# Performance work log

Hardware: AMD Instinct MI355X
Metric: run time of the kernel (lower is better)

Reference implementation:

```python
import jax, jax.numpy as jnp
import numpy as np

B, L, D = 16, 2048, 64

def setup_inputs() -> dict:
    key = jax.random.key(0)
    kq, kk, kv = jax.random.split(key, 3)
    q = jax.random.normal(kq, (B, L, D), dtype=jnp.float32)
    k = jax.random.normal(kk, (B, L, D), dtype=jnp.float32)
    v = jax.random.normal(kv, (B, L, D), dtype=jnp.float32)
    return {"q": q, "k": k, "v": v}

def reference(q, k, v):
    # scores: [B, L_q, L_k] = q @ k^T  (no scale applied, faithful to source)
    scores = jnp.einsum("bqd,bkd->bqk", q, k)
    attention = jax.nn.softmax(scores, axis=2)
    # dropout p=0.0 -> identity
    # source returns (v, attention), NOT the context
    return (v, attention)
```

## Files before the change

kernel.cpp:

```cpp
#include <hip/hip_runtime.h>
#include <hip/hip_bf16.h>

typedef short s16x8 __attribute__((ext_vector_type(8)));
typedef float f32x4 __attribute__((ext_vector_type(4)));

#define B_ 16
#define L_ 2048
#define D_ 64
#define V_ELEMS (B_ * L_ * D_)
#define MFMA16 __builtin_amdgcn_mfma_f32_16x16x32_bf16

__device__ __forceinline__ unsigned rne1(float f) {
    unsigned u = __builtin_bit_cast(unsigned, f);
    return (u + 0x7FFFu + ((u >> 16) & 1u)) >> 16;
}
__device__ __forceinline__ unsigned pack2(float a, float b) {
    return (rne1(a) & 0xFFFFu) | (rne1(b) << 16);
}
__device__ __forceinline__ unsigned cvtpk(float a, float b) {
    unsigned r;
    asm("v_cvt_pk_bf16_f32 %0, %1, %2" : "=v"(r) : "v"(a), "v"(b));
    return r;
}

__device__ __forceinline__ void split8(float4 a, float4 b, s16x8& hi, s16x8& lo) {
    float f[8] = {a.x, a.y, a.z, a.w, b.x, b.y, b.z, b.w};
    s16x8 h, l;
#pragma unroll
    for (int i = 0; i < 8; ++i) {
        unsigned u = __builtin_bit_cast(unsigned, f[i]);
        h[i] = (short)(u >> 16);
        float lf = f[i] - __builtin_bit_cast(float, u & 0xFFFF0000u);
        l[i] = (short)rne1(lf);
    }
    hi = h; lo = l;
}

__global__ void copy_v_kernel(const float4* __restrict__ v, float4* __restrict__ o) {
    int i = blockIdx.x * blockDim.x + threadIdx.x;
    o[i] = v[i];
}

__global__ void prep_qkv_kernel(const float4* __restrict__ q, const float4* __restrict__ k,
                                const float4* __restrict__ v,
                                uint2* __restrict__ qhi, uint2* __restrict__ qlo,
                                uint2* __restrict__ khi, uint2* __restrict__ klo,
                                float4* __restrict__ o) {
    int i = blockIdx.x * blockDim.x + threadIdx.x;
    o[i] = v[i];
    float4 fq = q[i];
    float4 fk = k[i];
    unsigned u0 = __builtin_bit_cast(unsigned, fq.x), u1 = __builtin_bit_cast(unsigned, fq.y);
    unsigned u2 = __builtin_bit_cast(unsigned, fq.z), u3 = __builtin_bit_cast(unsigned, fq.w);
    qhi[i] = make_uint2((u0 >> 16) | (u1 & 0xFFFF0000u), (u2 >> 16) | (u3 & 0xFFFF0000u));
    qlo[i] = make_uint2(
        pack2(fq.x - __builtin_bit_cast(float, u0 & 0xFFFF0000u),
              fq.y - __builtin_bit_cast(float, u1 & 0xFFFF0000u)),
        pack2(fq.z - __builtin_bit_cast(float, u2 & 0xFFFF0000u),
              fq.w - __builtin_bit_cast(float, u3 & 0xFFFF0000u)));
    u0 = __builtin_bit_cast(unsigned, fk.x); u1 = __builtin_bit_cast(unsigned, fk.y);
    u2 = __builtin_bit_cast(unsigned, fk.z); u3 = __builtin_bit_cast(unsigned, fk.w);
    khi[i] = make_uint2((u0 >> 16) | (u1 & 0xFFFF0000u), (u2 >> 16) | (u3 & 0xFFFF0000u));
    klo[i] = make_uint2(
        pack2(fk.x - __builtin_bit_cast(float, u0 & 0xFFFF0000u),
              fk.y - __builtin_bit_cast(float, u1 & 0xFFFF0000u)),
        pack2(fk.z - __builtin_bit_cast(float, u2 & 0xFFFF0000u),
              fk.w - __builtin_bit_cast(float, u3 & 0xFFFF0000u)));
}

__device__ __forceinline__ void store4nt(float* p, unsigned u0, unsigned u1, float inv) {
    f32x4 w;
    w[0] = __builtin_bit_cast(float, u0 << 16) * inv;
    w[1] = __builtin_bit_cast(float, u0 & 0xFFFF0000u) * inv;
    w[2] = __builtin_bit_cast(float, u1 << 16) * inv;
    w[3] = __builtin_bit_cast(float, u1 & 0xFFFF0000u) * inv;
    __builtin_nontemporal_store(w, (f32x4*)p);
}

template <bool PRE>
__global__ __launch_bounds__(1024, 4) void attn_kernel(
    const float* __restrict__ qf, const float* __restrict__ kf,
    const ushort* __restrict__ qhi, const ushort* __restrict__ qlo,
    const ushort* __restrict__ khi, const ushort* __restrict__ klo,
    float* __restrict__ og) {
    const int bid  = ((blockIdx.x & 7) << 7) | (blockIdx.x >> 3);
    const int b    = bid >> 6;
    const int q0   = (bid & 63) << 5;
    const int tid  = threadIdx.x;
    const int wave = tid >> 6;
    const int lane = tid & 63;
    const int nq   = lane & 15;
    const int quad = lane >> 4;

    s16x8 bhi[2][2], blo[2][2];
#pragma unroll
    for (int t = 0; t < 2; ++t) {
        const size_t off = ((size_t)(b * L_ + q0 + t * 16 + nq)) * D_ + quad * 8;
        if constexpr (PRE) {
            bhi[t][0] = *(const s16x8*)(qhi + off);
            bhi[t][1] = *(const s16x8*)(qhi + off + 32);
            blo[t][0] = *(const s16x8*)(qlo + off);
            blo[t][1] = *(const s16x8*)(qlo + off + 32);
        } else {
            float4 a0 = *(const float4*)(qf + off), a1 = *(const float4*)(qf + off + 4);
            float4 a2 = *(const float4*)(qf + off + 32), a3 = *(const float4*)(qf + off + 36);
            split8(a0, a1, bhi[t][0], blo[t][0]);
            split8(a2, a3, bhi[t][1], blo[t][1]);
        }
    }

    const size_t kbase = ((size_t)(b * L_ + wave * 128 + nq)) * D_ + quad * 8;
    const size_t tstep = (size_t)16 * D_;

    float s0 = 0.0f, s1 = 0.0f;
    unsigned pk0[16], pk1[16];

    s16x8 ah0, ah1, al0, al1;
    if constexpr (PRE) {
        ah0 = *(const s16x8*)(khi + kbase);
        ah1 = *(const s16x8*)(khi + kbase + 32);
        al0 = *(const s16x8*)(klo + kbase);
        al1 = *(const s16x8*)(klo + kbase + 32);
    } else {
        float4 a0 = *(const float4*)(kf + kbase), a1 = *(const float4*)(kf + kbase + 4);
        float4 a2 = *(const float4*)(kf + kbase + 32), a3 = *(const float4*)(kf + kbase + 36);
        split8(a0, a1, ah0, al0);
        split8(a2, a3, ah1, al1);
    }

#pragma unroll
    for (int t = 0; t < 8; ++t) {
        const size_t noff = kbase + (size_t)((t + 1) & 7) * tstep;
        s16x8 nh0, nh1, nl0, nl1;
        if constexpr (PRE) {
            nh0 = *(const s16x8*)(khi + noff);
            nh1 = *(const s16x8*)(khi + noff + 32);
            nl0 = *(const s16x8*)(klo + noff);
            nl1 = *(const s16x8*)(klo + noff + 32);
        } else {
            float4 a0 = *(const float4*)(kf + noff), a1 = *(const float4*)(kf + noff + 4);
            float4 a2 = *(const float4*)(kf + noff + 32), a3 = *(const float4*)(kf + noff + 36);
            split8(a0, a1, nh0, nl0);
            split8(a2, a3, nh1, nl1);
        }

        f32x4 c0 = {0.f, 0.f, 0.f, 0.f}, c1 = {0.f, 0.f, 0.f, 0.f};
        c0 = MFMA16(ah0, bhi[0][0], c0, 0, 0, 0);
        c1 = MFMA16(ah0, bhi[1][0], c1, 0, 0, 0);
        c0 = MFMA16(ah1, bhi[0][1], c0, 0, 0, 0);
        c1 = MFMA16(ah1, bhi[1][1], c1, 0, 0, 0);
        c0 = MFMA16(ah0, blo[0][0], c0, 0, 0, 0);
        c1 = MFMA16(ah0, blo[1][0], c1, 0, 0, 0);
        c0 = MFMA16(ah1, blo[0][1], c0, 0, 0, 0);
        c1 = MFMA16(ah1, blo[1][1], c1, 0, 0, 0);
        c0 = MFMA16(al0, bhi[0][0], c0, 0, 0, 0);
        c1 = MFMA16(al0, bhi[1][0], c1, 0, 0, 0);
        c0 = MFMA16(al1, bhi[0][1], c0, 0, 0, 0);
        c1 = MFMA16(al1, bhi[1][1], c1, 0, 0, 0);

        float e0 = __expf(c0[0]), e1 = __expf(c0[1]), e2 = __expf(c0[2]), e3 = __expf(c0[3]);
        s0 += (e0 + e1) + (e2 + e3);
        pk0[2 * t]     = cvtpk(e0, e1);
        pk0[2 * t + 1] = cvtpk(e2, e3);
        float g0 = __expf(c1[0]), g1 = __expf(c1[1]), g2 = __expf(c1[2]), g3 = __expf(c1[3]);
        s1 += (g0 + g1) + (g2 + g3);
        pk1[2 * t]     = cvtpk(g0, g1);
        pk1[2 * t + 1] = cvtpk(g2, g3);

        ah0 = nh0; ah1 = nh1; al0 = nl0; al1 = nl1;
    }

    s0 += __shfl_xor(s0, 16); s0 += __shfl_xor(s0, 32);
    s1 += __shfl_xor(s1, 16); s1 += __shfl_xor(s1, 32);
    __shared__ float wsum[16][2][16];
    if (lane < 16) { wsum[wave][0][lane] = s0; wsum[wave][1][lane] = s1; }
    __syncthreads();
    float t0 = 0.f, t1 = 0.f;
#pragma unroll
    for (int w = 0; w < 16; ++w) { t0 += wsum[w][0][nq]; t1 += wsum[w][1][nq]; }
    const float inv0 = 1.0f / t0;
    const float inv1 = 1.0f / t1;

    float* op0 = og + ((size_t)(b * L_ + q0 + nq)) * L_ + wave * 128 + quad * 4;
    float* op1 = op0 + (size_t)16 * L_;
#pragma unroll
    for (int t = 0; t < 8; ++t) {
        store4nt(op0 + t * 16, pk0[2 * t], pk0[2 * t + 1], inv0);
        store4nt(op1 + t * 16, pk1[2 * t], pk1[2 * t + 1], inv1);
    }
}

extern "C" void kernel_launch(void* const* d_in, const int* in_sizes, int n_in,
                              void* d_out, int out_size, void* d_ws, size_t ws_size,
                              hipStream_t stream) {
    const float* q = (const float*)d_in[0];
    const float* k = (const float*)d_in[1];
    const float* v = (const float*)d_in[2];
    float* out = (float*)d_out;

    float* att = out + (size_t)V_ELEMS;
    const size_t plane = (size_t)V_ELEMS;
    const size_t need  = 4 * plane * sizeof(ushort);
    ushort* qhi = (ushort*)d_ws;
    ushort* qlo = qhi + plane;
    ushort* khi = qlo + plane;
    ushort* klo = khi + plane;

    if (ws_size >= need) {
        prep_qkv_kernel<<<dim3(V_ELEMS / 4 / 256), dim3(256), 0, stream>>>(
            (const float4*)q, (const float4*)k, (const float4*)v,
            (uint2*)qhi, (uint2*)qlo, (uint2*)khi, (uint2*)klo, (float4*)out);
        attn_kernel<true><<<dim3(B_ * (L_ / 32)), dim3(1024), 0, stream>>>(
            q, k, qhi, qlo, khi, klo, att);
    } else {
        copy_v_kernel<<<dim3(V_ELEMS / 4 / 256), dim3(256), 0, stream>>>(
            (const float4*)v, (float4*)out);
        attn_kernel<false><<<dim3(B_ * (L_ / 32)), dim3(1024), 0, stream>>>(
            q, k, qhi, qlo, khi, klo, att);
    }
}
```

Baseline: 385.7 us.

## Stage packed softmax scores in LDS for coalesced row-contiguous output stores

The precomputed-split path now computes each 16-query half tile separately, writes the bf16-packed exponentials into a swizzled LDS stash, and then has the block write whole contiguous output rows with nontemporal float4 stores. Before, each lane wrote strided 16-byte pieces across rows. The aim is better coalescing on the 256MB attention output write, which is the dominant cost. In exchange, K is loaded twice (once per half tile), there are extra syncthreads and 128KB of LDS, and occupancy may drop.

New measurement: 404.5 us. 1.05x slower.

```diff
diff --git a/kernel.cpp b/kernel.cpp
--- a/kernel.cpp
+++ b/kernel.cpp
@@ -77,9 +77,7 @@
     __builtin_nontemporal_store(w, (f32x4*)p);
 }
 
-template <bool PRE>
-__global__ __launch_bounds__(1024, 4) void attn_kernel(
-    const float* __restrict__ qf, const float* __restrict__ kf,
+__global__ __launch_bounds__(1024, 4) void attn_lds_kernel(
     const ushort* __restrict__ qhi, const ushort* __restrict__ qlo,
     const ushort* __restrict__ khi, const ushort* __restrict__ klo,
     float* __restrict__ og) {
@@ -92,36 +90,113 @@
     const int nq   = lane & 15;
     const int quad = lane >> 4;
 
+    __shared__ unsigned stash[2][16][1024];
+    __shared__ float wsum[16][16];
+    __shared__ float inv_s[16];
+
     s16x8 bhi[2][2], blo[2][2];
 #pragma unroll
     for (int t = 0; t < 2; ++t) {
         const size_t off = ((size_t)(b * L_ + q0 + t * 16 + nq)) * D_ + quad * 8;
-        if constexpr (PRE) {
-            bhi[t][0] = *(const s16x8*)(qhi + off);
-            bhi[t][1] = *(const s16x8*)(qhi + off + 32);
-            blo[t][0] = *(const s16x8*)(qlo + off);
-            blo[t][1] = *(const s16x8*)(qlo + off + 32);
-        } else {
-            float4 a0 = *(const float4*)(qf + off), a1 = *(const float4*)(qf + off + 4);
-            float4 a2 = *(const float4*)(qf + off + 32), a3 = *(const float4*)(qf + off + 36);
-            split8(a0, a1, bhi[t][0], blo[t][0]);
-            split8(a2, a3, bhi[t][1], blo[t][1]);
-        }
+        bhi[t][0] = *(const s16x8*)(qhi + off);
+        bhi[t][1] = *(const s16x8*)(qhi + off + 32);
+        blo[t][0] = *(const s16x8*)(qlo + off);
+        blo[t][1] = *(const s16x8*)(qlo + off + 32);
     }
 
     const size_t kbase = ((size_t)(b * L_ + wave * 128 + nq)) * D_ + quad * 8;
     const size_t tstep = (size_t)16 * D_;
 
+    const int w3 = wave >> 3;
+    const int c4 = tid & 511;
+
+#pragma unroll
+    for (int tt = 0; tt < 2; ++tt) {
+        s16x8 ah0 = *(const s16x8*)(khi + kbase);
+        s16x8 ah1 = *(const s16x8*)(khi + kbase + 32);
+        s16x8 al0 = *(const s16x8*)(klo + kbase);
+        s16x8 al1 = *(const s16x8*)(klo + kbase + 32);
+
+        float s0 = 0.0f;
+#pragma unroll
+        for (int t = 0; t < 8; ++t) {
+            const size_t noff = kbase + (size_t)((t + 1) & 7) * tstep;
+            s16x8 nh0 = *(const s16x8*)(khi + noff);
+            s16x8 nh1 = *(const s16x8*)(khi + noff + 32);
+            s16x8 nl0 = *(const s16x8*)(klo + noff);
+            s16x8 nl1 = *(const s16x8*)(klo + noff + 32);
+
+            f32x4 c0 = {0.f, 0.f, 0.f, 0.f};
+            c0 = MFMA16(ah0, bhi[tt][0], c0, 0, 0, 0);
+            c0 = MFMA16(ah1, bhi[tt][1], c0, 0, 0, 0);
+            c0 = MFMA16(ah0, blo[tt][0], c0, 0, 0, 0);
+            c0 = MFMA16(ah1, blo[tt][1], c0, 0, 0, 0);
+            c0 = MFMA16(al0, bhi[tt][0], c0, 0, 0, 0);
+            c0 = MFMA16(al1, bhi[tt][1], c0, 0, 0, 0);
+
+            float e0 = __expf(c0[0]), e1 = __expf(c0[1]);
+            float e2 = __expf(c0[2]), e3 = __expf(c0[3]);
+            s0 += (e0 + e1) + (e2 + e3);
+            unsigned byteoff = ((unsigned)(wave * 64 + t * 8 + quad * 2) * 4u)
+                               ^ ((unsigned)nq << 3);
+            *(uint2*)((char*)&stash[tt][nq][0] + byteoff) =
+                make_uint2(cvtpk(e0, e1), cvtpk(e2, e3));
+
+            ah0 = nh0; ah1 = nh1; al0 = nl0; al1 = nl1;
+        }
+
+        s0 += __shfl_xor(s0, 16); s0 += __shfl_xor(s0, 32);
+        if (lane < 16) wsum[wave][nq] = s0;
+        __syncthreads();
+        if (tid < 16) {
+            float t0 = 0.f;
+#pragma unroll
+            for (int w = 0; w < 16; ++w) t0 += wsum[w][tid];
+            inv_s[tid] = 1.0f / t0;
+        }
+        __syncthreads();
+
+        float* obase = og + ((size_t)(b * L_ + q0 + tt * 16)) * L_;
+#pragma unroll
+        for (int p = 0; p < 8; ++p) {
+            const int r = 2 * p + w3;
+            unsigned byteoff = ((unsigned)c4 * 8u) ^ ((unsigned)r << 3);
+            uint2 u = *(const uint2*)((const char*)&stash[tt][r][0] + byteoff);
+            store4nt(obase + (size_t)r * L_ + (size_t)c4 * 4, u.x, u.y, inv_s[r]);
+        }
+    }
+}
+
+__global__ __launch_bounds__(1024, 4) void attn_fb_kernel(
+    const float* __restrict__ qf, const float* __restrict__ kf,
+    float* __restrict__ og) {
+    const int bid  = ((blockIdx.x & 7) << 7) | (blockIdx.x >> 3);
+    const int b    = bid >> 6;
+    const int q0   = (bid & 63) << 5;
+    const int tid  = threadIdx.x;
+    const int wave = tid >> 6;
+    const int lane = tid & 63;
+    const int nq   = lane & 15;
+    const int quad = lane >> 4;
+
+    s16x8 bhi[2][2], blo[2][2];
+#pragma unroll
+    for (int t = 0; t < 2; ++t) {
+        const size_t off = ((size_t)(b * L_ + q0 + t * 16 + nq)) * D_ + quad * 8;
+        float4 a0 = *(const float4*)(qf + off), a1 = *(const float4*)(qf + off + 4);
+        float4 a2 = *(const float4*)(qf + off + 32), a3 = *(const float4*)(qf + off + 36);
+        split8(a0, a1, bhi[t][0], blo[t][0]);
+        split8(a2, a3, bhi[t][1], blo[t][1]);
+    }
+
+    const size_t kbase = ((size_t)(b * L_ + wave * 128 + nq)) * D_ + quad * 8;
+    const size_t tstep = (size_t)16 * D_;
+
     float s0 = 0.0f, s1 = 0.0f;
     unsigned pk0[16], pk1[16];
 
     s16x8 ah0, ah1, al0, al1;
-    if constexpr (PRE) {
-        ah0 = *(const s16x8*)(khi + kbase);
-        ah1 = *(const s16x8*)(khi + kbase + 32);
-        al0 = *(const s16x8*)(klo + kbase);
-        al1 = *(const s16x8*)(klo + kbase + 32);
-    } else {
+    {
         float4 a0 = *(const float4*)(kf + kbase), a1 = *(const float4*)(kf + kbase + 4);
         float4 a2 = *(const float4*)(kf + kbase + 32), a3 = *(const float4*)(kf + kbase + 36);
         split8(a0, a1, ah0, al0);
@@ -132,18 +207,12 @@
     for (int t = 0; t < 8; ++t) {
         const size_t noff = kbase + (size_t)((t + 1) & 7) * tstep;
         s16x8 nh0, nh1, nl0, nl1;
-        if constexpr (PRE) {
-            nh0 = *(const s16x8*)(khi + noff);
-            nh1 = *(const s16x8*)(khi + noff + 32);
-            nl0 = *(const s16x8*)(klo + noff);
-            nl1 = *(const s16x8*)(klo + noff + 32);
-        } else {
+        {
             float4 a0 = *(const float4*)(kf + noff), a1 = *(const float4*)(kf + noff + 4);
             float4 a2 = *(const float4*)(kf + noff + 32), a3 = *(const float4*)(kf + noff + 36);
             split8(a0, a1, nh0, nl0);
             split8(a2, a3, nh1, nl1);
         }
-
         f32x4 c0 = {0.f, 0.f, 0.f, 0.f}, c1 = {0.f, 0.f, 0.f, 0.f};
         c0 = MFMA16(ah0, bhi[0][0], c0, 0, 0, 0);
         c1 = MFMA16(ah0, bhi[1][0], c1, 0, 0, 0);
@@ -160,12 +229,10 @@
 
         float e0 = __expf(c0[0]), e1 = __expf(c0[1]), e2 = __expf(c0[2]), e3 = __expf(c0[3]);
         s0 += (e0 + e1) + (e2 + e3);
-        pk0[2 * t]     = cvtpk(e0, e1);
-        pk0[2 * t + 1] = cvtpk(e2, e3);
+        pk0[2 * t] = cvtpk(e0, e1); pk0[2 * t + 1] = cvtpk(e2, e3);
         float g0 = __expf(c1[0]), g1 = __expf(c1[1]), g2 = __expf(c1[2]), g3 = __expf(c1[3]);
         s1 += (g0 + g1) + (g2 + g3);
-        pk1[2 * t]     = cvtpk(g0, g1);
-        pk1[2 * t + 1] = cvtpk(g2, g3);
+        pk1[2 * t] = cvtpk(g0, g1); pk1[2 * t + 1] = cvtpk(g2, g3);
 
         ah0 = nh0; ah1 = nh1; al0 = nl0; al1 = nl1;
     }
@@ -210,12 +277,12 @@
         prep_qkv_kernel<<<dim3(V_ELEMS / 4 / 256), dim3(256), 0, stream>>>(
             (const float4*)q, (const float4*)k, (const float4*)v,
             (uint2*)qhi, (uint2*)qlo, (uint2*)khi, (uint2*)klo, (float4*)out);
-        attn_kernel<true><<<dim3(B_ * (L_ / 32)), dim3(1024), 0, stream>>>(
-            q, k, qhi, qlo, khi, klo, att);
+        attn_lds_kernel<<<dim3(B_ * (L_ / 32)), dim3(1024), 0, stream>>>(
+            qhi, qlo, khi, klo, att);
     } else {
         copy_v_kernel<<<dim3(V_ELEMS / 4 / 256), dim3(256), 0, stream>>>(
             (const float4*)v, (float4*)out);
-        attn_kernel<false><<<dim3(B_ * (L_ / 32)), dim3(1024), 0, stream>>>(
-            q, k, qhi, qlo, khi, klo, att);
-    }
-}
+        attn_fb_kernel<<<dim3(B_ * (L_ / 32)), dim3(1024), 0, stream>>>(
+            q, k, att);
+    }
+}
```
